# Kernel tuning notes

Hardware: AMD Instinct MI355X
Metric: run time of the kernel (lower is better)

The kernel has to match this reference:

```python
import jax, jax.numpy as jnp
import numpy as np


def setup_inputs() -> dict:
    key = jax.random.key(0)
    k1, k2, k3 = jax.random.split(key, 3)
    B, C, F, T = 8, 64, 128, 2000
    mag_spec = jax.random.uniform(k1, (B, C, F, T), dtype=jnp.float32)
    initial_state = jax.random.uniform(k2, (B, C, F, 1), dtype=jnp.float32)
    weights = jax.random.uniform(k3, (C,), dtype=jnp.float32)  # per-channel smoothing
    return {"mag_spec": mag_spec, "initial_state": initial_state, "weights": weights}


def reference(mag_spec, initial_state, weights):
    # mag_spec: [B, C, F, T]; initial_state: [B, C, F, 1]; weights: [C]
    w = jnp.clip(weights, 0.0, 1.0)[:, None]  # [C, 1] broadcasts over (C, F)
    init = initial_state[..., 0]              # [B, C, F]

    def step(acc, x):  # x: [B, C, F]
        acc = w * x + (1.0 - w) * acc
        return acc, acc

    xs = jnp.moveaxis(mag_spec, -1, 0)         # [T, B, C, F]
    final, ys = jax.lax.scan(step, init, xs)   # ys: [T, B, C, F]
    out = jnp.moveaxis(ys, 0, -1)              # [B, C, F, T]
    return out, final[..., None]               # ([B,C,F,T], [B,C,F,1])
```

## Files before the change

### kernel.cpp

```cpp
#include <hip/hip_runtime.h>


#define T_LEN 2000
#define NROWS 65536
#define F_DIM 128
#define C_DIM 64

__global__ __launch_bounds__(256) void ema_scan_kernel(
    const float* __restrict__ x,
    const float* __restrict__ init,
    const float* __restrict__ weights,
    float* __restrict__ out,
    float* __restrict__ final_out)
{
    const int gwave = (blockIdx.x * blockDim.x + threadIdx.x) >> 6;
    const int lane  = threadIdx.x & 63;
    if (gwave >= NROWS) return;
    const int row = gwave;
    const int c   = (row >> 7) & (C_DIM - 1);

    float w = weights[c];
    w = fminf(fmaxf(w, 0.0f), 1.0f);
    const float a = 1.0f - w;

    const float a2   = a * a;
    const float a3   = a2 * a;
    const float a4   = a2 * a2;
    const float a8   = a4 * a4;
    const float a16  = a8 * a8;
    const float a32  = a16 * a16;
    const float a64  = a32 * a32;
    const float a128 = a64 * a64;
    const float a256 = a128 * a128;

    float pw = 1.0f;
    if (lane & 1)  pw *= a4;
    if (lane & 2)  pw *= a8;
    if (lane & 4)  pw *= a16;
    if (lane & 8)  pw *= a32;
    if (lane & 16) pw *= a64;
    if (lane & 32) pw *= a128;

    float acc = init[row];

    const float* __restrict__ xrow = x   + (long long)row * T_LEN;
    float* __restrict__       orow = out + (long long)row * T_LEN;

    #pragma unroll 1
    for (int t0 = 0; t0 < T_LEN; t0 += 256) {
        const int tl  = t0 + lane * 4;
        const int rem = T_LEN - tl;

        float x0 = 0.0f, x1 = 0.0f, x2 = 0.0f, x3 = 0.0f;
        if (rem >= 4) {
            const float4 v = *reinterpret_cast<const float4*>(xrow + tl);
            x0 = v.x; x1 = v.y; x2 = v.z; x3 = v.w;
        } else if (rem > 0) {
            x0 = xrow[tl];
            if (rem > 1) x1 = xrow[tl + 1];
            if (rem > 2) x2 = xrow[tl + 2];
        }

        float B = w * fmaf(a3, x0, fmaf(a2, x1, fmaf(a, x2, x3)));

        float Bup;
        Bup = __shfl_up(B, 1);  if (lane >= 1)  B = fmaf(a4,   Bup, B);
        Bup = __shfl_up(B, 2);  if (lane >= 2)  B = fmaf(a8,   Bup, B);
        Bup = __shfl_up(B, 4);  if (lane >= 4)  B = fmaf(a16,  Bup, B);
        Bup = __shfl_up(B, 8);  if (lane >= 8)  B = fmaf(a32,  Bup, B);
        Bup = __shfl_up(B, 16); if (lane >= 16) B = fmaf(a64,  Bup, B);
        Bup = __shfl_up(B, 32); if (lane >= 32) B = fmaf(a128, Bup, B);

        float Bexcl = __shfl_up(B, 1);
        if (lane == 0) Bexcl = 0.0f;

        float accl = fmaf(pw, acc, Bexcl);

        if (rem >= 4) {
            float4 o;
            accl = fmaf(a, accl, w * x0); o.x = accl;
            accl = fmaf(a, accl, w * x1); o.y = accl;
            accl = fmaf(a, accl, w * x2); o.z = accl;
            accl = fmaf(a, accl, w * x3); o.w = accl;
            *reinterpret_cast<float4*>(orow + tl) = o;
            if (tl + 4 == T_LEN) final_out[row] = accl;
        } else if (rem > 0) {
            accl = fmaf(a, accl, w * x0); orow[tl] = accl;
            if (rem > 1) { accl = fmaf(a, accl, w * x1); orow[tl + 1] = accl; }
            if (rem > 2) { accl = fmaf(a, accl, w * x2); orow[tl + 2] = accl; }
            final_out[row] = accl;
        }

        const float Btop = __shfl(B, 63);
        acc = fmaf(a256, acc, Btop);
    }
}

extern "C" void kernel_launch(void* const* d_in, const int* in_sizes, int n_in,
                              void* d_out, int out_size, void* d_ws, size_t ws_size,
                              hipStream_t stream) {
    const float* mag  = (const float*)d_in[0];
    const float* init = (const float*)d_in[1];
    const float* wgt  = (const float*)d_in[2];
    float* out = (float*)d_out;
    float* fin = out + (long long)NROWS * T_LEN;

    const int threads = 256;
    const int blocks  = NROWS / 4;
    ema_scan_kernel<<<blocks, threads, 0, stream>>>(mag, init, wgt, out, fin);
}
```

Baseline: 218.3 us.

## Preload whole row with nontemporal vector loads and fully unroll chunk loop

The kernel now issues all eight float4 loads for a row up front, then scans chunk by chunk, instead of loading one chunk per loop iteration. The loop is fully unrolled with a specialised tail chunk, which removes the per-lane remainder branches. Loads and stores use nontemporal builtins to bypass cache retention. This gives more memory-level parallelism per wave at the cost of more registers held live (32 floats of input), which may reduce occupancy.

```diff
diff --git a/kernel.cpp b/kernel.cpp
--- a/kernel.cpp
+++ b/kernel.cpp
@@ -1,10 +1,13 @@
 #include <hip/hip_runtime.h>
 
 
+typedef float f32x4 __attribute__((ext_vector_type(4)));
+
 #define T_LEN 2000
 #define NROWS 65536
-#define F_DIM 128
 #define C_DIM 64
+#define NCHUNK 8
+#define TAIL_LANES 52
 
 __global__ __launch_bounds__(256) void ema_scan_kernel(
     const float* __restrict__ x,
@@ -41,27 +44,30 @@
     if (lane & 16) pw *= a64;
     if (lane & 32) pw *= a128;
 
+    const float* __restrict__ xrow = x   + (long long)row * T_LEN;
+    float* __restrict__       orow = out + (long long)row * T_LEN;
+    const int tl = lane * 4;
+
+    f32x4 v[NCHUNK];
+    #pragma unroll
+    for (int i = 0; i < NCHUNK - 1; ++i)
+        v[i] = __builtin_nontemporal_load(
+                   reinterpret_cast<const f32x4*>(xrow + i * 256 + tl));
+    if (lane < TAIL_LANES)
+        v[NCHUNK - 1] = __builtin_nontemporal_load(
+                   reinterpret_cast<const f32x4*>(xrow + (NCHUNK - 1) * 256 + tl));
+    else {
+        f32x4 z = {0.0f, 0.0f, 0.0f, 0.0f};
+        v[NCHUNK - 1] = z;
+    }
+
     float acc = init[row];
 
-    const float* __restrict__ xrow = x   + (long long)row * T_LEN;
-    float* __restrict__       orow = out + (long long)row * T_LEN;
+    #pragma unroll
+    for (int i = 0; i < NCHUNK; ++i) {
+        const f32x4 xv = v[i];
 
-    #pragma unroll 1
-    for (int t0 = 0; t0 < T_LEN; t0 += 256) {
-        const int tl  = t0 + lane * 4;
-        const int rem = T_LEN - tl;
-
-        float x0 = 0.0f, x1 = 0.0f, x2 = 0.0f, x3 = 0.0f;
-        if (rem >= 4) {
-            const float4 v = *reinterpret_cast<const float4*>(xrow + tl);
-            x0 = v.x; x1 = v.y; x2 = v.z; x3 = v.w;
-        } else if (rem > 0) {
-            x0 = xrow[tl];
-            if (rem > 1) x1 = xrow[tl + 1];
-            if (rem > 2) x2 = xrow[tl + 2];
-        }
-
-        float B = w * fmaf(a3, x0, fmaf(a2, x1, fmaf(a, x2, x3)));
+        float B = w * fmaf(a3, xv.x, fmaf(a2, xv.y, fmaf(a, xv.z, xv.w)));
 
         float Bup;
         Bup = __shfl_up(B, 1);  if (lane >= 1)  B = fmaf(a4,   Bup, B);
@@ -76,23 +82,22 @@
 
         float accl = fmaf(pw, acc, Bexcl);
 
-        if (rem >= 4) {
-            float4 o;
-            accl = fmaf(a, accl, w * x0); o.x = accl;
-            accl = fmaf(a, accl, w * x1); o.y = accl;
-            accl = fmaf(a, accl, w * x2); o.z = accl;
-            accl = fmaf(a, accl, w * x3); o.w = accl;
-            *reinterpret_cast<float4*>(orow + tl) = o;
-            if (tl + 4 == T_LEN) final_out[row] = accl;
-        } else if (rem > 0) {
-            accl = fmaf(a, accl, w * x0); orow[tl] = accl;
-            if (rem > 1) { accl = fmaf(a, accl, w * x1); orow[tl + 1] = accl; }
-            if (rem > 2) { accl = fmaf(a, accl, w * x2); orow[tl + 2] = accl; }
-            final_out[row] = accl;
+        f32x4 o;
+        accl = fmaf(a, accl, w * xv.x); o.x = accl;
+        accl = fmaf(a, accl, w * xv.y); o.y = accl;
+        accl = fmaf(a, accl, w * xv.z); o.z = accl;
+        accl = fmaf(a, accl, w * xv.w); o.w = accl;
+
+        if (i < NCHUNK - 1) {
+            __builtin_nontemporal_store(o,
+                reinterpret_cast<f32x4*>(orow + i * 256 + tl));
+            const float Btop = __shfl(B, 63);
+            acc = fmaf(a256, acc, Btop);
+        } else if (lane < TAIL_LANES) {
+            __builtin_nontemporal_store(o,
+                reinterpret_cast<f32x4*>(orow + (NCHUNK - 1) * 256 + tl));
+            if (lane == TAIL_LANES - 1) final_out[row] = accl;
         }
-
-        const float Btop = __shfl(B, 63);
-        acc = fmaf(a256, acc, Btop);
     }
 }
 
```

New measurement: 180.4 us. 17.3% less time.
